# Performance work log

Measured on AMD Instinct MI355X. Metric: run time of the kernel, lower is better.

Reference implementation:

```python
import jax, jax.numpy as jnp
import numpy as np

EMBED_DIM = 512
N_HEADS = 8
D_K = EMBED_DIM // N_HEADS

def _xavier(key, shape):
    fan_in, fan_out = shape[1], shape[0]
    limit = np.sqrt(6.0 / (fan_in + fan_out))
    return jax.random.uniform(key, shape, jnp.float32, -limit, limit)

def setup_inputs() -> dict:
    key = jax.random.key(0)
    ks = jax.random.split(key, 8)
    B, S, D = 2, 4096, EMBED_DIM
    return {
        "q": jax.random.normal(ks[0], (B, S, D), jnp.float32),
        "k": jax.random.normal(ks[1], (B, S, D), jnp.float32),
        "v": jax.random.normal(ks[2], (B, S, D), jnp.float32),
        "W_q": _xavier(ks[3], (D, D)),
        "W_k": _xavier(ks[4], (D, D)),
        "W_v": _xavier(ks[5], (D, D)),
        "W_o": _xavier(ks[6], (D, D)),
        "b_o": jnp.zeros((D,), jnp.float32),
    }

def reference(q, k, v, W_q, W_k, W_v, W_o, b_o):
    B, Sq, D = q.shape
    Sk = k.shape[1]
    # linear projections (torch Linear: x @ W.T)
    qh = (q @ W_q.T).reshape(B, Sq, N_HEADS, D_K).transpose(0, 2, 1, 3)
    kh = (k @ W_k.T).reshape(B, Sk, N_HEADS, D_K).transpose(0, 2, 1, 3)
    vh = (v @ W_v.T).reshape(B, Sk, N_HEADS, D_K).transpose(0, 2, 1, 3)
    scores = jnp.einsum('bhqd,bhkd->bhqk', qh, kh)  # [B,H,Sq,Sk]
    causal = jnp.triu(jnp.ones((Sq, Sk), bool), k=1)
    scores = jnp.where(causal, -jnp.inf, scores)
    attn = jax.nn.softmax(scores / np.sqrt(D_K), axis=-1)
    ctx = jnp.einsum('bhqk,bhkd->bhqd', attn, vh)
    ctx = ctx.transpose(0, 2, 1, 3).reshape(B, Sq, D)
    return ctx @ W_o.T + b_o
```

## Files before the change

### kernel.cpp

```cpp
#include <hip/hip_runtime.h>

typedef _Float16 f16;
typedef _Float16 f16x8 __attribute__((ext_vector_type(8)));
typedef _Float16 f16x4 __attribute__((ext_vector_type(4)));
typedef _Float16 f16x2 __attribute__((ext_vector_type(2)));
typedef float f32x4 __attribute__((ext_vector_type(4)));
typedef float f32x16 __attribute__((ext_vector_type(16)));
typedef unsigned int u32x2 __attribute__((ext_vector_type(2)));

#define S_TOK 4096
#define NB 2
#define NH 8
#define DKH 64
#define DMODEL 512

static __device__ __forceinline__ f32x4 mfma16(f16x8 a, f16x8 b, f32x4 c) {
    return __builtin_amdgcn_mfma_f32_16x16x32_f16(a, b, c, 0, 0, 0);
}
static __device__ __forceinline__ f32x16 mfma32(f16x8 a, f16x8 b, f32x16 c) {
    return __builtin_amdgcn_mfma_f32_32x32x16_f16(a, b, c, 0, 0, 0);
}
static __device__ __forceinline__ void gl16(const f16* g, f16* l) {
    __builtin_amdgcn_global_load_lds(
        (const __attribute__((address_space(1))) unsigned int*)g,
        (__attribute__((address_space(3))) unsigned int*)l, 16, 0, 0);
}

__global__ __launch_bounds__(256)
void proj_fused_kernel(const float* __restrict__ qx, const float* __restrict__ kx,
                       const float* __restrict__ vx,
                       const float* __restrict__ Wqp, const float* __restrict__ Wkp,
                       const float* __restrict__ Wvp,
                       f16* __restrict__ qo, f16* __restrict__ ko, f16* __restrict__ vo)
{
    const int mode = blockIdx.z;
    const float* x = (mode == 0) ? qx : (mode == 1) ? kx : vx;
    const float* W = (mode == 0) ? Wqp : (mode == 1) ? Wkp : Wvp;
    f16* out = (mode == 0) ? qo : (mode == 1) ? ko : vo;

    __shared__ f16 As[128 * 40];
    __shared__ f16 Bs[128 * 40];
    const int m0 = blockIdx.x * 128;
    const int n0 = blockIdx.y * 128;
    const int tid = threadIdx.x;
    const int wv = tid >> 6;
    const int lane = tid & 63;
    const int lr = lane & 15, lg = lane >> 4;
    const int wm = (wv >> 1) * 64, wn = (wv & 1) * 64;

    f32x4 acc[4][4];
#pragma unroll
    for (int i = 0; i < 4; ++i)
#pragma unroll
        for (int j = 0; j < 4; ++j) acc[i][j] = f32x4{0.f, 0.f, 0.f, 0.f};

    for (int kb = 0; kb < DMODEL; kb += 32) {
#pragma unroll
        for (int c = 0; c < 2; ++c) {
            const int chunk = tid + c * 256;
            const int row = chunk >> 2;
            const int col = (chunk & 3) * 8;
            const float* ga = x + (size_t)(m0 + row) * DMODEL + kb + col;
            float4 a0 = *(const float4*)ga;
            float4 a1 = *(const float4*)(ga + 4);
            f16x8 ha = { (f16)a0.x, (f16)a0.y, (f16)a0.z, (f16)a0.w,
                         (f16)a1.x, (f16)a1.y, (f16)a1.z, (f16)a1.w };
            *(f16x8*)(As + row * 40 + col) = ha;
            const float* gb = W + (size_t)(n0 + row) * DMODEL + kb + col;
            float4 b0 = *(const float4*)gb;
            float4 b1 = *(const float4*)(gb + 4);
            f16x8 hb = { (f16)b0.x, (f16)b0.y, (f16)b0.z, (f16)b0.w,
                         (f16)b1.x, (f16)b1.y, (f16)b1.z, (f16)b1.w };
            *(f16x8*)(Bs + row * 40 + col) = hb;
        }
        __syncthreads();
        f16x8 af[4], bf[4];
#pragma unroll
        for (int i = 0; i < 4; ++i)
            af[i] = *(const f16x8*)(As + (wm + 16 * i + lr) * 40 + 8 * lg);
#pragma unroll
        for (int j = 0; j < 4; ++j)
            bf[j] = *(const f16x8*)(Bs + (wn + 16 * j + lr) * 40 + 8 * lg);
#pragma unroll
        for (int i = 0; i < 4; ++i)
#pragma unroll
            for (int j = 0; j < 4; ++j)
                acc[i][j] = mfma16(af[i], bf[j], acc[i][j]);
        __syncthreads();
    }

#pragma unroll
    for (int i = 0; i < 4; ++i) {
        const int mbase = m0 + wm + 16 * i + 4 * lg;
#pragma unroll
        for (int j = 0; j < 4; ++j) {
            const int n = n0 + wn + 16 * j + lr;
            const int h = n >> 6, dk = n & 63;
            if (mode == 2) {
                const int b = mbase >> 12;
                const int s = mbase & 4095;
                f16x4 v4;
#pragma unroll
                for (int r = 0; r < 4; ++r) v4[r] = (f16)acc[i][j][r];
                *(f16x4*)(out + ((size_t)(b * NH + h) * DKH + dk) * S_TOK + s) = v4;
            } else {
                const float sc = (mode == 0) ? 0.1803368801111244f : 1.0f;
#pragma unroll
                for (int r = 0; r < 4; ++r) {
                    const int m = mbase + r;
                    const int b = m >> 12, s = m & 4095;
                    out[((size_t)(b * NH + h) * S_TOK + s) * DKH + dk] = (f16)(acc[i][j][r] * sc);
                }
            }
        }
    }
}

__global__ __launch_bounds__(256, 4)
void attn_kernel(const f16* __restrict__ qh, const f16* __restrict__ kh,
                 const f16* __restrict__ vt, f16* __restrict__ pO, float* __restrict__ pL)
{
    __shared__ f16 Ks[2][64 * 64];
    __shared__ f16 Vs[2][64 * 64];

    const int bid = blockIdx.x;
    const int bh = 2 * (bid & 7) + ((bid >> 3) & 1);
    const int j = (bid >> 4) & 31;
    const int cb = (bid >> 9) & 1;
    const int tid = threadIdx.x, wv = tid >> 6, lane = tid & 63;
    const int l31 = lane & 31, h = lane >> 5;

    const f16* Qp = qh + (size_t)bh * S_TOK * DKH;
    const f16* Kp = kh + (size_t)bh * S_TOK * DKH;
    const f16* Vp = vt + (size_t)bh * DKH * S_TOK;

    const int srow = tid >> 3;
    const int sg = tid & 7;
    const int sgx = sg ^ (srow & 7);

    int cur = 0;
    for (int seg = 0; seg < 2; ++seg) {
        const int qt = seg ? (31 - j) : j;
        const int cc = seg ? (3 - cb) : cb;
        const int T = 2 * qt + 2;
        const int tb = (cc * T) >> 2;
        const int te = ((cc + 1) * T) >> 2;
        const int qw = qt * 128 + 32 * wv + l31;
        const int unit = (bh * 32 + qt) * 4 + cc;

        f16x8 aq[4];
#pragma unroll
        for (int s = 0; s < 4; ++s)
            aq[s] = *(const f16x8*)(Qp + (size_t)qw * DKH + 16 * s + 8 * h);

        f32x16 accO0 = {}, accO1 = {};
        float mrow = -1e20f, lrow = 0.f;

        if (te > tb) {
            {
                const f16* kp1 = Kp + (size_t)(64 * tb + srow) * DKH + sgx * 8;
                gl16(kp1, &Ks[cur][wv * 512]);
                gl16(kp1 + 32 * DKH, &Ks[cur][2048 + wv * 512]);
                const f16* vp1 = Vp + (size_t)srow * S_TOK + 64 * tb + sgx * 8;
                gl16(vp1, &Vs[cur][wv * 512]);
                gl16(vp1 + (size_t)32 * S_TOK, &Vs[cur][2048 + wv * 512]);
            }
            for (int t = tb; t < te; ++t) {
                __syncthreads();
                if (t + 1 < te) {
                    const f16* kp1 = Kp + (size_t)(64 * (t + 1) + srow) * DKH + sgx * 8;
                    gl16(kp1, &Ks[cur ^ 1][wv * 512]);
                    gl16(kp1 + 32 * DKH, &Ks[cur ^ 1][2048 + wv * 512]);
                    const f16* vp1 = Vp + (size_t)srow * S_TOK + 64 * (t + 1) + sgx * 8;
                    gl16(vp1, &Vs[cur ^ 1][wv * 512]);
                    gl16(vp1 + (size_t)32 * S_TOK, &Vs[cur ^ 1][2048 + wv * 512]);
                }
                const f16* Kb = &Ks[cur][0];
                const f16* Vb = &Vs[cur][0];

                f32x16 accS0 = {}, accS1 = {};
                __builtin_amdgcn_s_setprio(1);
#pragma unroll
                for (int s = 0; s < 4; ++s) {
                    f16x8 ak0 = *(const f16x8*)(Kb + l31 * 64 + ((2 * s + h) ^ (l31 & 7)) * 8);
                    f16x8 ak1 = *(const f16x8*)(Kb + (32 + l31) * 64 + ((2 * s + h) ^ (l31 & 7)) * 8);
                    accS0 = mfma32(ak0, aq[s], accS0);
                    accS1 = mfma32(ak1, aq[s], accS1);
                }
                __builtin_amdgcn_s_setprio(0);

                if (t >= 2 * qt) {
#pragma unroll
                    for (int e = 0; e < 16; ++e) {
                        const int kvb = 64 * t + (e & 3) + 8 * (e >> 2) + 4 * h;
                        accS0[e] = (kvb > qw) ? -1e30f : accS0[e];
                        accS1[e] = (kvb + 32 > qw) ? -1e30f : accS1[e];
                    }
                }

                float tm = -1e30f;
#pragma unroll
                for (int e = 0; e < 16; ++e) tm = fmaxf(tm, fmaxf(accS0[e], accS1[e]));
                tm = fmaxf(tm, __shfl_xor(tm, 32));
                if (!__all(tm <= mrow + 8.f)) {
                    const float mn = fmaxf(mrow, tm);
                    const float sf = exp2f(mrow - mn);
                    lrow *= sf;
                    accO0 *= sf;  accO1 *= sf;
                    mrow = mn;
                }

                float ts = 0.f;
                {
                    unsigned int Xd0[4], Xd1[4];
#pragma unroll
                    for (int g = 0; g < 4; ++g) {
                        float p0 = exp2f(accS0[4 * g + 0] - mrow);
                        float p1 = exp2f(accS0[4 * g + 1] - mrow);
                        float p2 = exp2f(accS0[4 * g + 2] - mrow);
                        float p3 = exp2f(accS0[4 * g + 3] - mrow);
                        ts += (p0 + p1) + (p2 + p3);
                        union { f16x2 hh; unsigned int u; } a0, a1;
                        a0.hh = f16x2{(f16)p0, (f16)p1};
                        a1.hh = f16x2{(f16)p2, (f16)p3};
                        Xd0[g] = a0.u;  Xd1[g] = a1.u;
                    }
                    __builtin_amdgcn_s_setprio(1);
#pragma unroll
                    for (int sp = 0; sp < 2; ++sp) {
                        u32x2 rA = __builtin_amdgcn_permlane32_swap(Xd0[2 * sp], Xd0[2 * sp + 1], false, false);
                        u32x2 rB = __builtin_amdgcn_permlane32_swap(Xd1[2 * sp], Xd1[2 * sp + 1], false, false);
                        union { unsigned int u[4]; f16x8 v; } F;
                        F.u[0] = rA[0]; F.u[1] = rB[0]; F.u[2] = rA[1]; F.u[3] = rB[1];
                        f16x8 av0 = *(const f16x8*)(Vb + l31 * 64 + ((2 * sp + h) ^ (l31 & 7)) * 8);
                        f16x8 av1 = *(const f16x8*)(Vb + (32 + l31) * 64 + ((2 * sp + h) ^ (l31 & 7)) * 8);
                        accO0 = mfma32(av0, F.v, accO0);
                        accO1 = mfma32(av1, F.v, accO1);
                    }
                    __builtin_amdgcn_s_setprio(0);
                }
                {
                    unsigned int Xd0[4], Xd1[4];
#pragma unroll
                    for (int g = 0; g < 4; ++g) {
                        float p0 = exp2f(accS1[4 * g + 0] - mrow);
                        float p1 = exp2f(accS1[4 * g + 1] - mrow);
                        float p2 = exp2f(accS1[4 * g + 2] - mrow);
                        float p3 = exp2f(accS1[4 * g + 3] - mrow);
                        ts += (p0 + p1) + (p2 + p3);
                        union { f16x2 hh; unsigned int u; } a0, a1;
                        a0.hh = f16x2{(f16)p0, (f16)p1};
                        a1.hh = f16x2{(f16)p2, (f16)p3};
                        Xd0[g] = a0.u;  Xd1[g] = a1.u;
                    }
                    __builtin_amdgcn_s_setprio(1);
#pragma unroll
                    for (int sp = 0; sp < 2; ++sp) {
                        const int spp = 2 + sp;
                        u32x2 rA = __builtin_amdgcn_permlane32_swap(Xd0[2 * sp], Xd0[2 * sp + 1], false, false);
                        u32x2 rB = __builtin_amdgcn_permlane32_swap(Xd1[2 * sp], Xd1[2 * sp + 1], false, false);
                        union { unsigned int u[4]; f16x8 v; } F;
                        F.u[0] = rA[0]; F.u[1] = rB[0]; F.u[2] = rA[1]; F.u[3] = rB[1];
                        f16x8 av0 = *(const f16x8*)(Vb + l31 * 64 + ((2 * spp + h) ^ (l31 & 7)) * 8);
                        f16x8 av1 = *(const f16x8*)(Vb + (32 + l31) * 64 + ((2 * spp + h) ^ (l31 & 7)) * 8);
                        accO0 = mfma32(av0, F.v, accO0);
                        accO1 = mfma32(av1, F.v, accO1);
                    }
                    __builtin_amdgcn_s_setprio(0);
                }
                ts += __shfl_xor(ts, 32);
                lrow += ts;
                cur ^= 1;
            }
        }

        const float invl = (lrow > 0.f) ? (1.f / lrow) : 0.f;
        f16* Ob = pO + ((size_t)unit * 128 + (32 * wv + l31)) * DKH;
#pragma unroll
        for (int g = 0; g < 4; ++g) {
            f16x4 o0, o1;
#pragma unroll
            for (int r = 0; r < 4; ++r) {
                o0[r] = (f16)(accO0[4 * g + r] * invl);
                o1[r] = (f16)(accO1[4 * g + r] * invl);
            }
            *(f16x4*)(Ob + 8 * g + 4 * h) = o0;
            *(f16x4*)(Ob + 32 + 8 * g + 4 * h) = o1;
        }
        if (h == 0)
            pL[unit * 128 + 32 * wv + l31] =
                (lrow > 0.f) ? (mrow + __log2f(lrow)) : -1e30f;
    }
}

__global__ __launch_bounds__(256)
void merge_kernel(const f16* __restrict__ pO, const float* __restrict__ pL,
                  f16* __restrict__ ctx)
{
    const int tid = threadIdx.x;
    const int R = blockIdx.x * 32 + (tid >> 3);
    const int dkg = tid & 7;
    const int bh = R >> 12, q = R & 4095;
    const int qt = q >> 7, qi = q & 127;
    const int ub = (bh * 32 + qt) * 4;

    float L[4];
#pragma unroll
    for (int c = 0; c < 4; ++c) L[c] = pL[(ub + c) * 128 + qi];
    float Lm = fmaxf(fmaxf(L[0], L[1]), fmaxf(L[2], L[3]));
    float w[4], wsum = 0.f;
#pragma unroll
    for (int c = 0; c < 4; ++c) { w[c] = exp2f(L[c] - Lm); wsum += w[c]; }
    const float inv = 1.f / wsum;

    float o[8];
#pragma unroll
    for (int i = 0; i < 8; ++i) o[i] = 0.f;
#pragma unroll
    for (int c = 0; c < 4; ++c) {
        f16x8 a = *(const f16x8*)(pO + ((size_t)(ub + c) * 128 + qi) * DKH + dkg * 8);
#pragma unroll
        for (int i = 0; i < 8; ++i) o[i] += w[c] * (float)a[i];
    }
    f16x8 ov;
#pragma unroll
    for (int i = 0; i < 8; ++i) ov[i] = (f16)(o[i] * inv);

    const int bb = bh >> 3, hh = bh & 7;
    *(f16x8*)(ctx + ((size_t)(bb * S_TOK + q)) * DMODEL + hh * DKH + dkg * 8) = ov;
}

__global__ __launch_bounds__(256)
void oproj_kernel(const f16* __restrict__ A, const float* __restrict__ W,
                  const float* __restrict__ bias, float* __restrict__ out)
{
    __shared__ f16 As[128 * 40];
    __shared__ f16 Bs[128 * 40];
    const int m0 = blockIdx.x * 128;
    const int n0 = blockIdx.y * 128;
    const int tid = threadIdx.x;
    const int wv = tid >> 6;
    const int lane = tid & 63;
    const int lr = lane & 15, lg = lane >> 4;
    const int wm = (wv >> 1) * 64, wn = (wv & 1) * 64;

    f32x4 acc[4][4];
#pragma unroll
    for (int i = 0; i < 4; ++i)
#pragma unroll
        for (int j = 0; j < 4; ++j) acc[i][j] = f32x4{0.f, 0.f, 0.f, 0.f};

    for (int kb = 0; kb < DMODEL; kb += 32) {
#pragma unroll
        for (int c = 0; c < 2; ++c) {
            const int chunk = tid + c * 256;
            const int row = chunk >> 2;
            const int col = (chunk & 3) * 8;
            *(f16x8*)(As + row * 40 + col) =
                *(const f16x8*)(A + (size_t)(m0 + row) * DMODEL + kb + col);
            const float* gb = W + (size_t)(n0 + row) * DMODEL + kb + col;
            float4 b0 = *(const float4*)gb;
            float4 b1 = *(const float4*)(gb + 4);
            f16x8 hb = { (f16)b0.x, (f16)b0.y, (f16)b0.z, (f16)b0.w,
                         (f16)b1.x, (f16)b1.y, (f16)b1.z, (f16)b1.w };
            *(f16x8*)(Bs + row * 40 + col) = hb;
        }
        __syncthreads();
        f16x8 af[4], bf[4];
#pragma unroll
        for (int i = 0; i < 4; ++i)
            af[i] = *(const f16x8*)(As + (wm + 16 * i + lr) * 40 + 8 * lg);
#pragma unroll
        for (int j = 0; j < 4; ++j)
            bf[j] = *(const f16x8*)(Bs + (wn + 16 * j + lr) * 40 + 8 * lg);
#pragma unroll
        for (int i = 0; i < 4; ++i)
#pragma unroll
            for (int j = 0; j < 4; ++j)
                acc[i][j] = mfma16(af[i], bf[j], acc[i][j]);
        __syncthreads();
    }

#pragma unroll
    for (int i = 0; i < 4; ++i) {
        const int mbase = m0 + wm + 16 * i + 4 * lg;
#pragma unroll
        for (int j = 0; j < 4; ++j) {
            const int n = n0 + wn + 16 * j + lr;
            const float bn = bias[n];
#pragma unroll
            for (int r = 0; r < 4; ++r) {
                const int m = mbase + r;
                out[(size_t)m * DMODEL + n] = acc[i][j][r] + bn;
            }
        }
    }
}

extern "C" void kernel_launch(void* const* d_in, const int* in_sizes, int n_in,
                              void* d_out, int out_size, void* d_ws, size_t ws_size,
                              hipStream_t stream) {
    const float* q  = (const float*)d_in[0];
    const float* k  = (const float*)d_in[1];
    const float* v  = (const float*)d_in[2];
    const float* Wq = (const float*)d_in[3];
    const float* Wk = (const float*)d_in[4];
    const float* Wv = (const float*)d_in[5];
    const float* Wo = (const float*)d_in[6];
    const float* bo = (const float*)d_in[7];
    float* out = (float*)d_out;

    const size_t per = (size_t)NB * NH * S_TOK * DKH;
    f16* qh  = (f16*)d_ws;
    f16* kh  = qh + per;
    f16* vt  = kh + per;
    f16* ctx = vt + per;
    f16* pO  = ctx + per;
    float* pL = (float*)(pO + (size_t)2048 * 128 * 64);

    proj_fused_kernel<<<dim3(64, 4, 3), 256, 0, stream>>>(q, k, v, Wq, Wk, Wv, qh, kh, vt);
    attn_kernel<<<dim3(1024), 256, 0, stream>>>(qh, kh, vt, pO, pL);
    merge_kernel<<<dim3(2048), 256, 0, stream>>>(pO, pL, ctx);
    oproj_kernel<<<dim3(64, 4), 256, 0, stream>>>(ctx, Wo, bo, out);
}
```

Before: 136.5 us.

## Split attention tile into two 32-key halves with online softmax and new LDS swizzle

Processes each 64-key tile as two 32-key halves, each doing QK MFMA, masking, max update, exp, and PV MFMA in sequence. This keeps only one S accumulator live instead of two, which lowers register pressure. The trade-off is an extra max reduction, rescale check, and cross-lane shuffle per tile. The LDS XOR swizzle also gains extra row-group bits for both the store and the K/V reads, aiming to reduce bank conflicts with the 32-row MFMA access pattern.

```diff
diff --git a/kernel.cpp b/kernel.cpp
--- a/kernel.cpp
+++ b/kernel.cpp
@@ -129,6 +129,7 @@
     const int cb = (bid >> 9) & 1;
     const int tid = threadIdx.x, wv = tid >> 6, lane = tid & 63;
     const int l31 = lane & 31, h = lane >> 5;
+    const int swzl = (l31 & 7) ^ (((l31 >> 3) & 3) << 1);
 
     const f16* Qp = qh + (size_t)bh * S_TOK * DKH;
     const f16* Kp = kh + (size_t)bh * S_TOK * DKH;
@@ -136,7 +137,7 @@
 
     const int srow = tid >> 3;
     const int sg = tid & 7;
-    const int sgx = sg ^ (srow & 7);
+    const int sgx = sg ^ ((srow & 7) ^ (((srow >> 3) & 3) << 1));
 
     int cur = 0;
     for (int seg = 0; seg < 2; ++seg) {
@@ -177,99 +178,75 @@
                 }
                 const f16* Kb = &Ks[cur][0];
                 const f16* Vb = &Vs[cur][0];
-
-                f32x16 accS0 = {}, accS1 = {};
-                __builtin_amdgcn_s_setprio(1);
-#pragma unroll
-                for (int s = 0; s < 4; ++s) {
-                    f16x8 ak0 = *(const f16x8*)(Kb + l31 * 64 + ((2 * s + h) ^ (l31 & 7)) * 8);
-                    f16x8 ak1 = *(const f16x8*)(Kb + (32 + l31) * 64 + ((2 * s + h) ^ (l31 & 7)) * 8);
-                    accS0 = mfma32(ak0, aq[s], accS0);
-                    accS1 = mfma32(ak1, aq[s], accS1);
-                }
-                __builtin_amdgcn_s_setprio(0);
-
-                if (t >= 2 * qt) {
-#pragma unroll
-                    for (int e = 0; e < 16; ++e) {
-                        const int kvb = 64 * t + (e & 3) + 8 * (e >> 2) + 4 * h;
-                        accS0[e] = (kvb > qw) ? -1e30f : accS0[e];
-                        accS1[e] = (kvb + 32 > qw) ? -1e30f : accS1[e];
+                const bool diag = (t >= 2 * qt);
+
+#pragma unroll
+                for (int half = 0; half < 2; ++half) {
+                    f32x16 accS = {};
+                    __builtin_amdgcn_s_setprio(1);
+#pragma unroll
+                    for (int s = 0; s < 4; ++s) {
+                        f16x8 ak = *(const f16x8*)(Kb + (32 * half + l31) * 64 +
+                                                   ((2 * s + h) ^ swzl) * 8);
+                        accS = mfma32(ak, aq[s], accS);
                     }
-                }
-
-                float tm = -1e30f;
-#pragma unroll
-                for (int e = 0; e < 16; ++e) tm = fmaxf(tm, fmaxf(accS0[e], accS1[e]));
-                tm = fmaxf(tm, __shfl_xor(tm, 32));
-                if (!__all(tm <= mrow + 8.f)) {
-                    const float mn = fmaxf(mrow, tm);
-                    const float sf = exp2f(mrow - mn);
-                    lrow *= sf;
-                    accO0 *= sf;  accO1 *= sf;
-                    mrow = mn;
-                }
-
-                float ts = 0.f;
-                {
+                    __builtin_amdgcn_s_setprio(0);
+
+                    if (diag) {
+#pragma unroll
+                        for (int e = 0; e < 16; ++e) {
+                            const int kvb = 64 * t + 32 * half + (e & 3) + 8 * (e >> 2) + 4 * h;
+                            accS[e] = (kvb > qw) ? -1e30f : accS[e];
+                        }
+                    }
+
+                    float m8a = fmaxf(fmaxf(accS[0], accS[1]), fmaxf(accS[2], accS[3]));
+                    float m8b = fmaxf(fmaxf(accS[4], accS[5]), fmaxf(accS[6], accS[7]));
+                    float m8c = fmaxf(fmaxf(accS[8], accS[9]), fmaxf(accS[10], accS[11]));
+                    float m8d = fmaxf(fmaxf(accS[12], accS[13]), fmaxf(accS[14], accS[15]));
+                    float tm = fmaxf(fmaxf(m8a, m8b), fmaxf(m8c, m8d));
+                    tm = fmaxf(tm, __shfl_xor(tm, 32));
+                    if (!__all(tm <= mrow + 8.f)) {
+                        const float mn = fmaxf(mrow, tm);
+                        const float sf = exp2f(mrow - mn);
+                        lrow *= sf;
+                        accO0 *= sf;  accO1 *= sf;
+                        mrow = mn;
+                    }
+
                     unsigned int Xd0[4], Xd1[4];
+                    float ts4[4];
 #pragma unroll
                     for (int g = 0; g < 4; ++g) {
-                        float p0 = exp2f(accS0[4 * g + 0] - mrow);
-                        float p1 = exp2f(accS0[4 * g + 1] - mrow);
-                        float p2 = exp2f(accS0[4 * g + 2] - mrow);
-                        float p3 = exp2f(accS0[4 * g + 3] - mrow);
-                        ts += (p0 + p1) + (p2 + p3);
+                        float p0 = exp2f(accS[4 * g + 0] - mrow);
+                        float p1 = exp2f(accS[4 * g + 1] - mrow);
+                        float p2 = exp2f(accS[4 * g + 2] - mrow);
+                        float p3 = exp2f(accS[4 * g + 3] - mrow);
+                        ts4[g] = (p0 + p1) + (p2 + p3);
                         union { f16x2 hh; unsigned int u; } a0, a1;
                         a0.hh = f16x2{(f16)p0, (f16)p1};
                         a1.hh = f16x2{(f16)p2, (f16)p3};
                         Xd0[g] = a0.u;  Xd1[g] = a1.u;
                     }
+                    float ts = (ts4[0] + ts4[1]) + (ts4[2] + ts4[3]);
+                    ts += __shfl_xor(ts, 32);
+                    lrow += ts;
+
                     __builtin_amdgcn_s_setprio(1);
 #pragma unroll
                     for (int sp = 0; sp < 2; ++sp) {
+                        const int spp = 2 * half + sp;
                         u32x2 rA = __builtin_amdgcn_permlane32_swap(Xd0[2 * sp], Xd0[2 * sp + 1], false, false);
                         u32x2 rB = __builtin_amdgcn_permlane32_swap(Xd1[2 * sp], Xd1[2 * sp + 1], false, false);
                         union { unsigned int u[4]; f16x8 v; } F;
                         F.u[0] = rA[0]; F.u[1] = rB[0]; F.u[2] = rA[1]; F.u[3] = rB[1];
-                        f16x8 av0 = *(const f16x8*)(Vb + l31 * 64 + ((2 * sp + h) ^ (l31 & 7)) * 8);
-                        f16x8 av1 = *(const f16x8*)(Vb + (32 + l31) * 64 + ((2 * sp + h) ^ (l31 & 7)) * 8);
+                        f16x8 av0 = *(const f16x8*)(Vb + l31 * 64 + ((2 * spp + h) ^ swzl) * 8);
+                        f16x8 av1 = *(const f16x8*)(Vb + (32 + l31) * 64 + ((2 * spp + h) ^ swzl) * 8);
                         accO0 = mfma32(av0, F.v, accO0);
                         accO1 = mfma32(av1, F.v, accO1);
                     }
                     __builtin_amdgcn_s_setprio(0);
                 }
-                {
-                    unsigned int Xd0[4], Xd1[4];
-#pragma unroll
-                    for (int g = 0; g < 4; ++g) {
-                        float p0 = exp2f(accS1[4 * g + 0] - mrow);
-                        float p1 = exp2f(accS1[4 * g + 1] - mrow);
-                        float p2 = exp2f(accS1[4 * g + 2] - mrow);
-                        float p3 = exp2f(accS1[4 * g + 3] - mrow);
-                        ts += (p0 + p1) + (p2 + p3);
-                        union { f16x2 hh; unsigned int u; } a0, a1;
-                        a0.hh = f16x2{(f16)p0, (f16)p1};
-                        a1.hh = f16x2{(f16)p2, (f16)p3};
-                        Xd0[g] = a0.u;  Xd1[g] = a1.u;
-                    }
-                    __builtin_amdgcn_s_setprio(1);
-#pragma unroll
-                    for (int sp = 0; sp < 2; ++sp) {
-                        const int spp = 2 + sp;
-                        u32x2 rA = __builtin_amdgcn_permlane32_swap(Xd0[2 * sp], Xd0[2 * sp + 1], false, false);
-                        u32x2 rB = __builtin_amdgcn_permlane32_swap(Xd1[2 * sp], Xd1[2 * sp + 1], false, false);
-                        union { unsigned int u[4]; f16x8 v; } F;
-                        F.u[0] = rA[0]; F.u[1] = rB[0]; F.u[2] = rA[1]; F.u[3] = rB[1];
-                        f16x8 av0 = *(const f16x8*)(Vb + l31 * 64 + ((2 * spp + h) ^ (l31 & 7)) * 8);
-                        f16x8 av1 = *(const f16x8*)(Vb + (32 + l31) * 64 + ((2 * spp + h) ^ (l31 & 7)) * 8);
-                        accO0 = mfma32(av0, F.v, accO0);
-                        accO1 = mfma32(av1, F.v, accO1);
-                    }
-                    __builtin_amdgcn_s_setprio(0);
-                }
-                ts += __shfl_xor(ts, 32);
-                lrow += ts;
                 cur ^= 1;
             }
         }
```

New measurement: 131.7 us. 1.04x faster.
